# Optimization experiments

Measured on AMD Instinct MI355X. Metric: run time of the kernel, lower is better.

The kernel has to match this reference:

```python
import jax, jax.numpy as jnp
import numpy as np
from jax import lax

B, C, XH, XW, KH, KW = 32, 128, 96, 96, 3, 3
BN_EPS = 1e-5


def setup_inputs() -> dict:
    key = jax.random.key(0)
    k1, k2, k3 = jax.random.split(key, 3)
    x = jax.random.normal(k1, (B, C, XH, XW), dtype=jnp.float32)
    k = jax.random.normal(k2, (B, C, KH, KW), dtype=jnp.float32)
    pw_weight = jax.random.normal(k3, (C, C), dtype=jnp.float32) * (1.0 / np.sqrt(C))
    bn_gamma = jnp.ones((C,), dtype=jnp.float32)
    bn_beta = jnp.zeros((C,), dtype=jnp.float32)
    bn_mean = jnp.zeros((C,), dtype=jnp.float32)
    bn_var = jnp.ones((C,), dtype=jnp.float32)
    return {"x": x, "k": k, "pw_weight": pw_weight, "bn_gamma": bn_gamma,
            "bn_beta": bn_beta, "bn_mean": bn_mean, "bn_var": bn_var}


def _depthwise_one(xi, ki):
    # xi: [C, XH, XW], ki: [C, KH, KW] -> per-sample depthwise conv, padding=KH//2
    pad = KH // 2
    out = lax.conv_general_dilated(
        xi[None],                 # [1, C, XH, XW]
        ki[:, None],              # [C, 1, KH, KW]  (OIHW with groups=C)
        window_strides=(1, 1),
        padding=((pad, pad), (pad, pad)),
        feature_group_count=C,
        dimension_numbers=("NCHW", "OIHW", "NCHW"),
    )
    return out[0]


def reference(x, k, pw_weight, bn_gamma, bn_beta, bn_mean, bn_var):
    # Per-sample dynamic depthwise conv, batched via vmap (replaces the Python loop)
    x_new = jax.vmap(_depthwise_one)(x, k)          # [B, C, XH, XW]
    # 1x1 pointwise conv (no bias)
    y = jnp.einsum("bchw,oc->bohw", x_new, pw_weight)
    # BatchNorm (inference form with running stats) + ReLU
    inv = bn_gamma * lax.rsqrt(bn_var + BN_EPS)
    y = y * inv[None, :, None, None] + (bn_beta - bn_mean * inv)[None, :, None, None]
    return jax.nn.relu(y)
```

## Files before the change

### kernel.cpp

```cpp
#include <hip/hip_runtime.h>
#include <hip/hip_bf16.h>

#define BB 32
#define CC 128
#define HH 96
#define WW 96
#define BN_EPS 1e-5f

typedef __attribute__((ext_vector_type(8))) short bf16x8_t;
typedef __attribute__((ext_vector_type(4))) float f32x4_t;
typedef __attribute__((ext_vector_type(4), aligned(4))) float f32x4u_t;
typedef __attribute__((ext_vector_type(2))) unsigned int u32x2_t;
typedef __attribute__((ext_vector_type(4))) unsigned int u32x4_t;

typedef const float __attribute__((address_space(1))) gfloat_t;
typedef float __attribute__((address_space(3))) sfloat_t;

__global__ __launch_bounds__(256)
void prep_kernel(const float* __restrict__ pw,
                 const float* __restrict__ g, const float* __restrict__ b,
                 const float* __restrict__ m, const float* __restrict__ v,
                 unsigned short* __restrict__ wper,
                 float* __restrict__ inv, float* __restrict__ bias)
{
    int t = blockIdx.x * 256 + threadIdx.x;
    if (t < CC * CC) {
        int o = t >> 7, cidx = t & 127;
        int kc = cidx >> 5, r = cidx & 31, gg = r >> 3, j = r & 7;
        int c = kc * 32 + gg * 4 + (j & 3) + 16 * (j >> 2);
        __hip_bfloat16 h = __float2bfloat16(pw[o * CC + c]);
        wper[o * CC + cidx] = *reinterpret_cast<unsigned short*>(&h);
    }
    if (t < CC) {
        float iv = g[t] * rsqrtf(v[t] + BN_EPS);
        inv[t] = iv;
        bias[t] = b[t] - m[t] * iv;
    }
}

__global__ __launch_bounds__(256, 6)
void dw_kernel(const float* __restrict__ x, const float* __restrict__ kk,
               unsigned short* __restrict__ xn)
{
    __shared__ __align__(16) float tile[2][18 * 96];
    const int tid = threadIdx.x;

    const unsigned wg  = blockIdx.x;
    const unsigned bid = (wg & 7u) * 512u + (wg >> 3);
    const int cs = bid & 127;
    const int b  = bid >> 7;

    const int kc = cs >> 5, rr2 = cs & 31, gg = rr2 >> 3, jj = rr2 & 7;
    const int c = kc * 32 + gg * 4 + (jj & 3) + 16 * (jj >> 2);

    const float* plane = x + (size_t)(b * CC + c) * (HH * WW);
    unsigned short* xplane = xn + (size_t)(b * CC + cs) * (HH * WW);

    const float* kp = kk + (size_t)(b * CC + c) * 9;
    const float kw0 = kp[0], kw1 = kp[1], kw2 = kp[2];
    const float kw3 = kp[3], kw4 = kp[4], kw5 = kp[5];
    const float kw6 = kp[6], kw7 = kp[7], kw8 = kp[8];

    const int rowA = tid / 24;
    const int colA = (tid % 24) * 4;
    const int sB   = tid + 256;
    const int rowB = sB / 24;
    const int colB = (sB % 24) * 4;
    const bool hasB = (sB < 432);

    auto STAGE = [&](int t, int buf) {
        int hA = t * 16 - 1 + rowA;
        hA = hA < 0 ? 0 : (hA > HH - 1 ? HH - 1 : hA);
        __builtin_amdgcn_global_load_lds(
            (gfloat_t*)(plane + (size_t)hA * WW + colA),
            (sfloat_t*)&tile[buf][tid * 4], 16, 0, 0);
        if (hasB) {
            int hB = t * 16 - 1 + rowB;
            hB = hB < 0 ? 0 : (hB > HH - 1 ? HH - 1 : hB);
            __builtin_amdgcn_global_load_lds(
                (gfloat_t*)(plane + (size_t)hB * WW + colB),
                (sfloat_t*)&tile[buf][sB * 4], 16, 0, 0);
        }
    };

    const int r  = tid >> 4;
    const int cc = (tid & 15) * 6;

    auto COMPUTE = [&](int buf, int t) {
        float v[3][8];
        #pragma unroll
        for (int dr = 0; dr < 3; ++dr) {
            const float* trow = &tile[buf][(r + dr) * 96];
            const float lv = trow[cc == 0 ? 0 : cc - 1];
            v[dr][0] = (cc == 0) ? 0.f : lv;
            #pragma unroll
            for (int i = 0; i < 6; ++i) v[dr][1 + i] = trow[cc + i];
            const float rv = trow[cc == 90 ? 95 : cc + 6];
            v[dr][7] = (cc == 90) ? 0.f : rv;
        }
        if (t == 0 && r == 0) {
            #pragma unroll
            for (int i = 0; i < 8; ++i) v[0][i] = 0.f;
        }
        if (t == 5 && r == 15) {
            #pragma unroll
            for (int i = 0; i < 8; ++i) v[2][i] = 0.f;
        }
        unsigned pk[3];
        #pragma unroll
        for (int pr = 0; pr < 3; ++pr) {
            const int j0 = 2 * pr, j1 = j0 + 1;
            float s0 = v[0][j0] * kw0;
            s0 = fmaf(v[0][j0 + 1], kw1, s0);
            s0 = fmaf(v[0][j0 + 2], kw2, s0);
            s0 = fmaf(v[1][j0],     kw3, s0);
            s0 = fmaf(v[1][j0 + 1], kw4, s0);
            s0 = fmaf(v[1][j0 + 2], kw5, s0);
            s0 = fmaf(v[2][j0],     kw6, s0);
            s0 = fmaf(v[2][j0 + 1], kw7, s0);
            s0 = fmaf(v[2][j0 + 2], kw8, s0);
            float s1 = v[0][j1] * kw0;
            s1 = fmaf(v[0][j1 + 1], kw1, s1);
            s1 = fmaf(v[0][j1 + 2], kw2, s1);
            s1 = fmaf(v[1][j1],     kw3, s1);
            s1 = fmaf(v[1][j1 + 1], kw4, s1);
            s1 = fmaf(v[1][j1 + 2], kw5, s1);
            s1 = fmaf(v[2][j1],     kw6, s1);
            s1 = fmaf(v[2][j1 + 1], kw7, s1);
            s1 = fmaf(v[2][j1 + 2], kw8, s1);
            __hip_bfloat16 h0b = __float2bfloat16(s0);
            __hip_bfloat16 h1b = __float2bfloat16(s1);
            pk[pr] = (unsigned)*reinterpret_cast<unsigned short*>(&h0b)
                   | ((unsigned)*reinterpret_cast<unsigned short*>(&h1b) << 16);
        }
        unsigned short* dst = xplane + (size_t)(t * 16 + r) * WW + cc;
        *reinterpret_cast<unsigned*>(dst)     = pk[0];
        *reinterpret_cast<unsigned*>(dst + 2) = pk[1];
        *reinterpret_cast<unsigned*>(dst + 4) = pk[2];
    };

    STAGE(0, 0);
    __syncthreads();
    STAGE(1, 1);

    #pragma unroll
    for (int t = 0; t < 6; ++t) {
        COMPUTE(t & 1, t);
        __syncthreads();
        if (t + 2 < 6) STAGE(t + 2, t & 1);
    }
}

__global__ __launch_bounds__(256, 3)
void pw_kernel(const unsigned short* __restrict__ xn,
               const unsigned short* __restrict__ wper,
               const float* __restrict__ invp, const float* __restrict__ biasp,
               float* __restrict__ out)
{
    __shared__ __align__(16) unsigned char xnb[128 * 256];
    const int tid = threadIdx.x;

    const unsigned wg  = blockIdx.x;
    const unsigned nid = (wg & 7u) * 96u + (wg >> 3);
    const int tw  = nid % 6u;
    const int thg = (nid / 6u) % 4u;
    const int b   = nid / 24u;
    const int w0  = tw * 16;

    const int lane   = tid & 63;
    const int wv     = tid >> 6;
    const int lo     = lane & 15;
    const int hi     = lane >> 4;
    const int o_base = wv * 32;

    bf16x8_t wfrag[2][4];
    #pragma unroll
    for (int t2 = 0; t2 < 2; ++t2)
        #pragma unroll
        for (int kc = 0; kc < 4; ++kc)
            wfrag[t2][kc] = *reinterpret_cast<const bf16x8_t*>(
                wper + (size_t)(o_base + t2 * 16 + lo) * CC + kc * 32 + hi * 8);

    float iv2[2], bs2[2];
    #pragma unroll
    for (int t2 = 0; t2 < 2; ++t2) {
        iv2[t2] = invp[o_base + t2 * 16 + lo];
        bs2[t2] = biasp[o_base + t2 * 16 + lo];
    }

    const int cs4 = tid >> 3;
    const int py  = tid & 7;
    const unsigned short* src_base =
        xn + (size_t)(b * CC + cs4 * 4) * (HH * WW) + (size_t)py * WW + w0;

    unsigned dLA[4][4], dRA[4][4], dLB[4][4], dRB[4][4];

    auto LOADREGS = [&](int t, unsigned (*dL)[4], unsigned (*dR)[4]) {
        const unsigned short* s0 = src_base + (size_t)((thg * 3 + t) * 8) * WW;
        #pragma unroll
        for (int q = 0; q < 4; ++q) {
            const unsigned short* src = s0 + (size_t)q * (HH * WW);
            u32x4_t L = *(const u32x4_t*)src;
            u32x4_t R = *(const u32x4_t*)(src + 8);
            dL[q][0]=L.x; dL[q][1]=L.y; dL[q][2]=L.z; dL[q][3]=L.w;
            dR[q][0]=R.x; dR[q][1]=R.y; dR[q][2]=R.z; dR[q][3]=R.w;
        }
    };

    auto WRITE_LDS = [&](unsigned (*dL)[4], unsigned (*dR)[4]) {
        #pragma unroll
        for (int o8 = 0; o8 < 2; ++o8) {
            #pragma unroll
            for (int j = 0; j < 4; ++j) {
                const unsigned d0 = o8 ? dR[0][j] : dL[0][j];
                const unsigned d1 = o8 ? dR[1][j] : dL[1][j];
                const unsigned d2 = o8 ? dR[2][j] : dL[2][j];
                const unsigned d3 = o8 ? dR[3][j] : dL[3][j];
                u32x2_t we, wo;
                we.x = __builtin_amdgcn_perm(d1, d0, 0x05040100u);
                we.y = __builtin_amdgcn_perm(d3, d2, 0x05040100u);
                wo.x = __builtin_amdgcn_perm(d1, d0, 0x07060302u);
                wo.y = __builtin_amdgcn_perm(d3, d2, 0x07060302u);
                const int pe = py * 16 + o8 * 8 + 2 * j;
                const int po = pe + 1;
                *reinterpret_cast<u32x2_t*>(&xnb[(unsigned)pe * 256 +
                    (((unsigned)cs4 * 8) ^ (((unsigned)pe & 7u) << 4))]) = we;
                *reinterpret_cast<u32x2_t*>(&xnb[(unsigned)po * 256 +
                    (((unsigned)cs4 * 8) ^ (((unsigned)po & 7u) << 4))]) = wo;
            }
        }
    };

    auto COMPUTE = [&](int t) {
        const int h0 = (thg * 3 + t) * 8;
        f32x4_t acc[8][2];
        #pragma unroll
        for (int pt = 0; pt < 8; ++pt) {
            acc[pt][0] = (f32x4_t){0.f, 0.f, 0.f, 0.f};
            acc[pt][1] = (f32x4_t){0.f, 0.f, 0.f, 0.f};
        }
        #pragma unroll
        for (int pt = 0; pt < 8; ++pt) {
            const unsigned rowbase = (unsigned)(pt * 16 + lo) * 256;
            const unsigned sw = (unsigned)((lo & 7) << 4);
            #pragma unroll
            for (int kc = 0; kc < 4; ++kc) {
                bf16x8_t xfrag = *reinterpret_cast<const bf16x8_t*>(
                    &xnb[rowbase + (((unsigned)(kc * 64 + hi * 16)) ^ sw)]);
                acc[pt][0] = __builtin_amdgcn_mfma_f32_16x16x32_bf16(
                    xfrag, wfrag[0][kc], acc[pt][0], 0, 0, 0);
                acc[pt][1] = __builtin_amdgcn_mfma_f32_16x16x32_bf16(
                    xfrag, wfrag[1][kc], acc[pt][1], 0, 0, 0);
            }
        }
        #pragma unroll
        for (int pt = 0; pt < 8; ++pt) {
            const int hrow = h0 + pt;
            #pragma unroll
            for (int t2 = 0; t2 < 2; ++t2) {
                const int o = o_base + t2 * 16 + lo;
                f32x4_t vv;
                #pragma unroll
                for (int rix = 0; rix < 4; ++rix)
                    vv[rix] = fmaxf(fmaf(acc[pt][t2][rix], iv2[t2], bs2[t2]), 0.f);
                __builtin_nontemporal_store(vv, reinterpret_cast<f32x4_t*>(
                    out + ((size_t)(b * CC + o) * HH + hrow) * WW + w0 + hi * 4));
            }
        }
    };

    LOADREGS(0, dLA, dRA);
    WRITE_LDS(dLA, dRA);
    LOADREGS(1, dLB, dRB);
    __syncthreads();
    COMPUTE(0);
    __syncthreads();
    WRITE_LDS(dLB, dRB);
    LOADREGS(2, dLA, dRA);
    __syncthreads();
    COMPUTE(1);
    __syncthreads();
    WRITE_LDS(dLA, dRA);
    __syncthreads();
    COMPUTE(2);
}

__global__ __launch_bounds__(256, 3)
void fused_main(const float* __restrict__ x, const float* __restrict__ kk,
                const unsigned short* __restrict__ wper,
                const float* __restrict__ invp, const float* __restrict__ biasp,
                float* __restrict__ out)
{
    __shared__ __align__(16) unsigned char xnb[128 * 256];
    const int tid = threadIdx.x;
    const unsigned wg  = blockIdx.x;
    const unsigned nid = (wg & 7u) * 288u + (wg >> 3);
    const int bx = nid % 6u;
    const int by = (nid / 6u) % 12u;
    const int bb = nid / 72u;
    const int w0 = bx * 16;
    const int h0 = by * 8;
    {
        const int wq = tid & 3;
        const int cp = tid >> 2;
        const int s  = cp << 1;
        const int kc = s >> 5, rr = s & 31, gg = rr >> 3, jj = rr & 7;
        const int cA = kc * 32 + gg * 4 + (jj & 3) + 16 * (jj >> 2);
        const int gw = w0 + wq * 4;
        const bool l_edge = (gw == 0);
        const bool r_edge = (gw + 4 >= WW);
        const float* planeA = x + (size_t)(bb * CC + cA) * (HH * WW);
        float kwA[9], kwB[9];
        {
            const float* kp = kk + (size_t)(bb * CC + cA) * 9;
            f32x4u_t q0 = *(const f32x4u_t*)(kp + 0);
            f32x4u_t q1 = *(const f32x4u_t*)(kp + 4);
            f32x4u_t q2 = *(const f32x4u_t*)(kp + 8);
            f32x4u_t q3 = *(const f32x4u_t*)(kp + 12);
            float     e16 = kp[16], e17 = kp[17];
            kwA[0]=q0.x; kwA[1]=q0.y; kwA[2]=q0.z; kwA[3]=q0.w;
            kwA[4]=q1.x; kwA[5]=q1.y; kwA[6]=q1.z; kwA[7]=q1.w;
            kwA[8]=q2.x;
            kwB[0]=q2.y; kwB[1]=q2.z; kwB[2]=q2.w;
            kwB[3]=q3.x; kwB[4]=q3.y; kwB[5]=q3.z; kwB[6]=q3.w;
            kwB[7]=e16;  kwB[8]=e17;
        }
        float xd[2][10][6];
        #pragma unroll
        for (int q = 0; q < 2; ++q) {
            const float* plane = planeA + q * (HH * WW);
            #pragma unroll
            for (int r = 0; r < 10; ++r) {
                const int row = h0 - 1 + r;
                const bool valid = (row >= 0) && (row < HH);
                const int rrow = row < 0 ? 0 : (row >= HH ? HH - 1 : row);
                const float* rp = plane + rrow * WW + gw;
                f32x4_t M = *(const f32x4_t*)rp;
                float vl = rp[l_edge ? 0 : -1];
                float vr = rp[r_edge ? 3 : 4];
                xd[q][r][0] = (valid && !l_edge) ? vl : 0.f;
                xd[q][r][1] = valid ? M.x : 0.f;
                xd[q][r][2] = valid ? M.y : 0.f;
                xd[q][r][3] = valid ? M.z : 0.f;
                xd[q][r][4] = valid ? M.w : 0.f;
                xd[q][r][5] = (valid && !r_edge) ? vr : 0.f;
            }
        }
        #pragma unroll
        for (int py = 0; py < 8; ++py) {
            #pragma unroll
            for (int i = 0; i < 4; ++i) {
                float sA = 0.f, sB = 0.f;
                #pragma unroll
                for (int t = 0; t < 3; ++t) {
                    sA = fmaf(xd[0][py + 0][i + t], kwA[t],     sA);
                    sA = fmaf(xd[0][py + 1][i + t], kwA[3 + t], sA);
                    sA = fmaf(xd[0][py + 2][i + t], kwA[6 + t], sA);
                    sB = fmaf(xd[1][py + 0][i + t], kwB[t],     sB);
                    sB = fmaf(xd[1][py + 1][i + t], kwB[3 + t], sB);
                    sB = fmaf(xd[1][py + 2][i + t], kwB[6 + t], sB);
                }
                __hip_bfloat16 hA = __float2bfloat16(sA);
                __hip_bfloat16 hB = __float2bfloat16(sB);
                unsigned pk = (unsigned)*reinterpret_cast<unsigned short*>(&hA)
                            | ((unsigned)*reinterpret_cast<unsigned short*>(&hB) << 16);
                const int p = py * 16 + wq * 4 + i;
                const unsigned boff = ((unsigned)(cp << 2)) ^ (((unsigned)p & 7u) << 4);
                *reinterpret_cast<unsigned*>(&xnb[(unsigned)p * 256 + boff]) = pk;
            }
        }
    }
    __syncthreads();
    {
        const int lane   = tid & 63;
        const int wv     = tid >> 6;
        const int lo     = lane & 15;
        const int hi     = lane >> 4;
        const int o_base = wv * 32;
        bf16x8_t afrag[2][4];
        #pragma unroll
        for (int t2 = 0; t2 < 2; ++t2)
            #pragma unroll
            for (int kc = 0; kc < 4; ++kc)
                afrag[t2][kc] = *reinterpret_cast<const bf16x8_t*>(
                    wper + (size_t)(o_base + t2 * 16 + lo) * CC + kc * 32 + hi * 8);
        f32x4_t acc[8][2];
        #pragma unroll
        for (int pt = 0; pt < 8; ++pt) {
            acc[pt][0] = (f32x4_t){0.f, 0.f, 0.f, 0.f};
            acc[pt][1] = (f32x4_t){0.f, 0.f, 0.f, 0.f};
        }
        #pragma unroll
        for (int pt = 0; pt < 8; ++pt) {
            const unsigned rowbase = (unsigned)(pt * 16 + lo) * 256;
            const unsigned sw = (unsigned)((lo & 7) << 4);
            #pragma unroll
            for (int kc = 0; kc < 4; ++kc) {
                bf16x8_t bfrag = *reinterpret_cast<const bf16x8_t*>(
                    &xnb[rowbase + (((unsigned)(kc * 64 + hi * 16)) ^ sw)]);
                acc[pt][0] = __builtin_amdgcn_mfma_f32_16x16x32_bf16(
                    afrag[0][kc], bfrag, acc[pt][0], 0, 0, 0);
                acc[pt][1] = __builtin_amdgcn_mfma_f32_16x16x32_bf16(
                    afrag[1][kc], bfrag, acc[pt][1], 0, 0, 0);
            }
        }
        float iv[2][4], bs[2][4];
        #pragma unroll
        for (int t2 = 0; t2 < 2; ++t2)
            #pragma unroll
            for (int r = 0; r < 4; ++r) {
                const int o = o_base + t2 * 16 + hi * 4 + r;
                iv[t2][r] = invp[o];
                bs[t2][r] = biasp[o];
            }
        #pragma unroll
        for (int pt = 0; pt < 8; ++pt) {
            const int hrow = h0 + pt;
            #pragma unroll
            for (int t2 = 0; t2 < 2; ++t2) {
                #pragma unroll
                for (int r = 0; r < 4; ++r) {
                    const int o = o_base + t2 * 16 + hi * 4 + r;
                    float val = fmaf(acc[pt][t2][r], iv[t2][r], bs[t2][r]);
                    val = fmaxf(val, 0.f);
                    out[((size_t)(bb * CC + o) * HH + hrow) * WW + w0 + lo] = val;
                }
            }
        }
    }
}

extern "C" void kernel_launch(void* const* d_in, const int* in_sizes, int n_in,
                              void* d_out, int out_size, void* d_ws, size_t ws_size,
                              hipStream_t stream) {
    const float* x   = (const float*)d_in[0];
    const float* kk  = (const float*)d_in[1];
    const float* pwt = (const float*)d_in[2];
    const float* g   = (const float*)d_in[3];
    const float* b   = (const float*)d_in[4];
    const float* m   = (const float*)d_in[5];
    const float* v   = (const float*)d_in[6];
    float* out = (float*)d_out;

    unsigned short* wper = (unsigned short*)d_ws;
    float* inv  = (float*)((char*)d_ws + 32768);
    float* bias = (float*)((char*)d_ws + 32768 + 512);
    unsigned short* xn = (unsigned short*)((char*)d_ws + 36864);
    const size_t need = 36864 + (size_t)BB * CC * HH * WW * 2;

    prep_kernel<<<64, 256, 0, stream>>>(pwt, g, b, m, v, wper, inv, bias);
    if (ws_size >= need) {
        dw_kernel<<<dim3(4096), 256, 0, stream>>>(x, kk, xn);
        pw_kernel<<<dim3(768), 256, 0, stream>>>(xn, wper, inv, bias, out);
    } else {
        fused_main<<<dim3(2304), 256, 0, stream>>>(x, kk, wper, inv, bias, out);
    }
}
```

Before: 94.55 us.

## Give each wavefront its own channel plane in depthwise kernel, fold prep in

The depthwise kernel now assigns one (batch, channel) plane per wavefront instead of per workgroup. Each wave stages its own 8-row tiles into a private XOR-swizzled LDS buffer, so block-wide __syncthreads can be replaced by explicit waitcnt fences. Threads compute 12 outputs per row with vectorized LDS reads and 8-byte stores. The separate prep kernel is folded into the first blocks of the depthwise launch, which removes one kernel launch. The risk is that pw_kernel consumes wper/inv/bias written by the previous kernel, which relies on stream ordering; that remains valid.

```diff
diff --git a/kernel.cpp b/kernel.cpp
--- a/kernel.cpp
+++ b/kernel.cpp
@@ -38,17 +38,41 @@
     }
 }
 
-__global__ __launch_bounds__(256, 6)
+__global__ __launch_bounds__(256, 5)
 void dw_kernel(const float* __restrict__ x, const float* __restrict__ kk,
+               const float* __restrict__ pwt,
+               const float* __restrict__ bng, const float* __restrict__ bnb,
+               const float* __restrict__ bnm, const float* __restrict__ bnv,
+               unsigned short* __restrict__ wper,
+               float* __restrict__ invp, float* __restrict__ biasp,
                unsigned short* __restrict__ xn)
 {
-    __shared__ __align__(16) float tile[2][18 * 96];
-    const int tid = threadIdx.x;
+    __shared__ __align__(16) float tile[4][2][960];
+    const int tid  = threadIdx.x;
+    const int wv   = tid >> 6;
+    const int lane = tid & 63;
+
+    {
+        const int t = blockIdx.x * 256 + tid;
+        if (t < CC * CC) {
+            int o = t >> 7, cidx = t & 127;
+            int kc2 = cidx >> 5, r2 = cidx & 31, g2 = r2 >> 3, j2 = r2 & 7;
+            int c2 = kc2 * 32 + g2 * 4 + (j2 & 3) + 16 * (j2 >> 2);
+            __hip_bfloat16 h = __float2bfloat16(pwt[o * CC + c2]);
+            wper[o * CC + cidx] = *reinterpret_cast<unsigned short*>(&h);
+        }
+        if (t < CC) {
+            float iv = bng[t] * rsqrtf(bnv[t] + BN_EPS);
+            invp[t] = iv;
+            biasp[t] = bnb[t] - bnm[t] * iv;
+        }
+    }
 
     const unsigned wg  = blockIdx.x;
-    const unsigned bid = (wg & 7u) * 512u + (wg >> 3);
-    const int cs = bid & 127;
-    const int b  = bid >> 7;
+    const unsigned bid = (wg & 7u) * 128u + (wg >> 3);
+    const int p  = (int)bid * 4 + wv;
+    const int cs = p & 127;
+    const int b  = p >> 7;
 
     const int kc = cs >> 5, rr2 = cs & 31, gg = rr2 >> 3, jj = rr2 & 7;
     const int c = kc * 32 + gg * 4 + (jj & 3) + 16 * (jj >> 2);
@@ -61,93 +85,108 @@
     const float kw3 = kp[3], kw4 = kp[4], kw5 = kp[5];
     const float kw6 = kp[6], kw7 = kp[7], kw8 = kp[8];
 
-    const int rowA = tid / 24;
-    const int colA = (tid % 24) * 4;
-    const int sB   = tid + 256;
-    const int rowB = sB / 24;
-    const int colB = (sB % 24) * 4;
-    const bool hasB = (sB < 432);
-
     auto STAGE = [&](int t, int buf) {
-        int hA = t * 16 - 1 + rowA;
-        hA = hA < 0 ? 0 : (hA > HH - 1 ? HH - 1 : hA);
-        __builtin_amdgcn_global_load_lds(
-            (gfloat_t*)(plane + (size_t)hA * WW + colA),
-            (sfloat_t*)&tile[buf][tid * 4], 16, 0, 0);
-        if (hasB) {
-            int hB = t * 16 - 1 + rowB;
-            hB = hB < 0 ? 0 : (hB > HH - 1 ? HH - 1 : hB);
-            __builtin_amdgcn_global_load_lds(
-                (gfloat_t*)(plane + (size_t)hB * WW + colB),
-                (sfloat_t*)&tile[buf][sB * 4], 16, 0, 0);
+        #pragma unroll
+        for (int q = 0; q < 4; ++q) {
+            const int slot = q * 64 + lane;
+            if (slot < 240) {
+                const int row = slot / 24;
+                const int sl  = slot % 24;
+                const int ssl = sl ^ (row & 7);
+                int xr = t * 8 - 1 + row;
+                xr = xr < 0 ? 0 : (xr > HH - 1 ? HH - 1 : xr);
+                __builtin_amdgcn_global_load_lds(
+                    (gfloat_t*)(plane + (size_t)xr * WW + ssl * 4),
+                    (sfloat_t*)&tile[wv][buf][q * 256 + lane * 4], 16, 0, 0);
+            }
         }
     };
 
-    const int r  = tid >> 4;
-    const int cc = (tid & 15) * 6;
+    const int r  = lane >> 3;
+    const int cg = lane & 7;
+    const int cc = cg * 12;
 
     auto COMPUTE = [&](int buf, int t) {
-        float v[3][8];
+        const float* tb = tile[wv][buf];
+        float w[3][14];
         #pragma unroll
         for (int dr = 0; dr < 3; ++dr) {
-            const float* trow = &tile[buf][(r + dr) * 96];
-            const float lv = trow[cc == 0 ? 0 : cc - 1];
-            v[dr][0] = (cc == 0) ? 0.f : lv;
-            #pragma unroll
-            for (int i = 0; i < 6; ++i) v[dr][1 + i] = trow[cc + i];
-            const float rv = trow[cc == 90 ? 95 : cc + 6];
-            v[dr][7] = (cc == 90) ? 0.f : rv;
+            const int rw  = r + dr;
+            const int key = rw & 7;
+            const int base = rw * 96;
+            f32x4_t a0 = *(const f32x4_t*)&tb[base + (((3 * cg)     ^ key) << 2)];
+            f32x4_t a1 = *(const f32x4_t*)&tb[base + (((3 * cg + 1) ^ key) << 2)];
+            f32x4_t a2 = *(const f32x4_t*)&tb[base + (((3 * cg + 2) ^ key) << 2)];
+            float lv = tb[base + (((cg == 0 ? 0 : 3 * cg - 1) ^ key) << 2) + 3];
+            float rv = tb[base + (((cg == 7 ? 23 : 3 * cg + 3) ^ key) << 2) +
+                          (cg == 7 ? 3 : 0)];
+            w[dr][0]  = (cg == 0) ? 0.f : lv;
+            w[dr][1]  = a0.x; w[dr][2]  = a0.y; w[dr][3]  = a0.z; w[dr][4]  = a0.w;
+            w[dr][5]  = a1.x; w[dr][6]  = a1.y; w[dr][7]  = a1.z; w[dr][8]  = a1.w;
+            w[dr][9]  = a2.x; w[dr][10] = a2.y; w[dr][11] = a2.z; w[dr][12] = a2.w;
+            w[dr][13] = (cg == 7) ? 0.f : rv;
         }
         if (t == 0 && r == 0) {
             #pragma unroll
-            for (int i = 0; i < 8; ++i) v[0][i] = 0.f;
-        }
-        if (t == 5 && r == 15) {
-            #pragma unroll
-            for (int i = 0; i < 8; ++i) v[2][i] = 0.f;
-        }
-        unsigned pk[3];
-        #pragma unroll
-        for (int pr = 0; pr < 3; ++pr) {
+            for (int i = 0; i < 14; ++i) w[0][i] = 0.f;
+        }
+        if (t == 11 && r == 7) {
+            #pragma unroll
+            for (int i = 0; i < 14; ++i) w[2][i] = 0.f;
+        }
+        unsigned pk[6];
+        #pragma unroll
+        for (int pr = 0; pr < 6; ++pr) {
             const int j0 = 2 * pr, j1 = j0 + 1;
-            float s0 = v[0][j0] * kw0;
-            s0 = fmaf(v[0][j0 + 1], kw1, s0);
-            s0 = fmaf(v[0][j0 + 2], kw2, s0);
-            s0 = fmaf(v[1][j0],     kw3, s0);
-            s0 = fmaf(v[1][j0 + 1], kw4, s0);
-            s0 = fmaf(v[1][j0 + 2], kw5, s0);
-            s0 = fmaf(v[2][j0],     kw6, s0);
-            s0 = fmaf(v[2][j0 + 1], kw7, s0);
-            s0 = fmaf(v[2][j0 + 2], kw8, s0);
-            float s1 = v[0][j1] * kw0;
-            s1 = fmaf(v[0][j1 + 1], kw1, s1);
-            s1 = fmaf(v[0][j1 + 2], kw2, s1);
-            s1 = fmaf(v[1][j1],     kw3, s1);
-            s1 = fmaf(v[1][j1 + 1], kw4, s1);
-            s1 = fmaf(v[1][j1 + 2], kw5, s1);
-            s1 = fmaf(v[2][j1],     kw6, s1);
-            s1 = fmaf(v[2][j1 + 1], kw7, s1);
-            s1 = fmaf(v[2][j1 + 2], kw8, s1);
+            float s0 = w[0][j0] * kw0;
+            s0 = fmaf(w[0][j0 + 1], kw1, s0);
+            s0 = fmaf(w[0][j0 + 2], kw2, s0);
+            s0 = fmaf(w[1][j0],     kw3, s0);
+            s0 = fmaf(w[1][j0 + 1], kw4, s0);
+            s0 = fmaf(w[1][j0 + 2], kw5, s0);
+            s0 = fmaf(w[2][j0],     kw6, s0);
+            s0 = fmaf(w[2][j0 + 1], kw7, s0);
+            s0 = fmaf(w[2][j0 + 2], kw8, s0);
+            float s1 = w[0][j1] * kw0;
+            s1 = fmaf(w[0][j1 + 1], kw1, s1);
+            s1 = fmaf(w[0][j1 + 2], kw2, s1);
+            s1 = fmaf(w[1][j1],     kw3, s1);
+            s1 = fmaf(w[1][j1 + 1], kw4, s1);
+            s1 = fmaf(w[1][j1 + 2], kw5, s1);
+            s1 = fmaf(w[2][j1],     kw6, s1);
+            s1 = fmaf(w[2][j1 + 1], kw7, s1);
+            s1 = fmaf(w[2][j1 + 2], kw8, s1);
             __hip_bfloat16 h0b = __float2bfloat16(s0);
             __hip_bfloat16 h1b = __float2bfloat16(s1);
             pk[pr] = (unsigned)*reinterpret_cast<unsigned short*>(&h0b)
                    | ((unsigned)*reinterpret_cast<unsigned short*>(&h1b) << 16);
         }
-        unsigned short* dst = xplane + (size_t)(t * 16 + r) * WW + cc;
-        *reinterpret_cast<unsigned*>(dst)     = pk[0];
-        *reinterpret_cast<unsigned*>(dst + 2) = pk[1];
-        *reinterpret_cast<unsigned*>(dst + 4) = pk[2];
+        unsigned short* dst = xplane + (size_t)(t * 8 + r) * WW + cc;
+        u32x2_t v01; v01.x = pk[0]; v01.y = pk[1];
+        u32x2_t v23; v23.x = pk[2]; v23.y = pk[3];
+        u32x2_t v45; v45.x = pk[4]; v45.y = pk[5];
+        *reinterpret_cast<u32x2_t*>(dst)     = v01;
+        *reinterpret_cast<u32x2_t*>(dst + 4) = v23;
+        *reinterpret_cast<u32x2_t*>(dst + 8) = v45;
     };
 
     STAGE(0, 0);
-    __syncthreads();
+    asm volatile("s_waitcnt vmcnt(0)" ::: "memory");
+    __builtin_amdgcn_sched_barrier(0);
     STAGE(1, 1);
 
     #pragma unroll
-    for (int t = 0; t < 6; ++t) {
+    for (int t = 0; t < 12; ++t) {
         COMPUTE(t & 1, t);
-        __syncthreads();
-        if (t + 2 < 6) STAGE(t + 2, t & 1);
+        asm volatile("s_waitcnt lgkmcnt(0)" ::: "memory");
+        __builtin_amdgcn_sched_barrier(0);
+        if (t + 2 < 12) {
+            STAGE(t + 2, t & 1);
+            asm volatile("s_waitcnt vmcnt(4)" ::: "memory");
+        } else {
+            asm volatile("s_waitcnt vmcnt(0)" ::: "memory");
+        }
+        __builtin_amdgcn_sched_barrier(0);
     }
 }
 
@@ -448,11 +487,12 @@
     unsigned short* xn = (unsigned short*)((char*)d_ws + 36864);
     const size_t need = 36864 + (size_t)BB * CC * HH * WW * 2;
 
-    prep_kernel<<<64, 256, 0, stream>>>(pwt, g, b, m, v, wper, inv, bias);
     if (ws_size >= need) {
-        dw_kernel<<<dim3(4096), 256, 0, stream>>>(x, kk, xn);
+        dw_kernel<<<dim3(1024), 256, 0, stream>>>(x, kk, pwt, g, b, m, v,
+                                                  wper, inv, bias, xn);
         pw_kernel<<<dim3(768), 256, 0, stream>>>(xn, wper, inv, bias, out);
     } else {
+        prep_kernel<<<64, 256, 0, stream>>>(pwt, g, b, m, v, wper, inv, bias);
         fused_main<<<dim3(2304), 256, 0, stream>>>(x, kk, wper, inv, bias, out);
     }
 }
```

Result: no change. 93.20 us (-1.4%).
